# Performance work log

Hardware: AMD Instinct MI355X
Metric: run time of the kernel (lower is better)

## Reference

```python
import jax, jax.numpy as jnp
import numpy as np

NQ = 4  # n_qubits_per_head


def _apply_ry(state, theta, q):
    # state: (N, 2,2,2,2) real amplitudes; theta: (N,) per-element angle; wire q
    st = jnp.moveaxis(state, 1 + q, -1)
    c = jnp.cos(0.5 * theta).reshape(-1, 1, 1, 1)
    s = jnp.sin(0.5 * theta).reshape(-1, 1, 1, 1)
    a0, a1 = st[..., 0], st[..., 1]
    st = jnp.stack([c * a0 - s * a1, s * a0 + c * a1], axis=-1)
    return jnp.moveaxis(st, -1, 1 + q)


def _apply_cnot(state, ctrl, tgt):
    st = jnp.moveaxis(state, (1 + ctrl, 1 + tgt), (-2, -1))
    st = jnp.stack([st[..., 0, :], st[..., 1, ::-1]], axis=-2)
    return jnp.moveaxis(st, (-2, -1), (1 + ctrl, 1 + tgt))


def _quantum_circuit(x_in, par):
    # x_in: (N, NQ) data angles; par: (N, L, NQ) variational angles (per head, tiled)
    N = x_in.shape[0]
    L = par.shape[1]
    state = jnp.zeros((N, 2, 2, 2, 2), x_in.dtype).at[:, 0, 0, 0, 0].set(1.0)
    for l in range(L):
        for q in range(NQ):
            state = _apply_ry(state, par[:, l, q], q)
        for q in range(NQ - 1):
            state = _apply_cnot(state, q, q + 1)
        state = _apply_cnot(state, NQ - 1, 0)
    for q in range(NQ):
        state = _apply_ry(state, x_in[:, q], q)
    p = state * state  # probabilities (real amplitudes: only RY/CNOT gates)
    zs = []
    for q in range(NQ):
        st = jnp.moveaxis(p, 1 + q, -1)
        zs.append(jnp.sum(st[..., 0], axis=(1, 2, 3)) - jnp.sum(st[..., 1], axis=(1, 2, 3)))
    return jnp.stack(zs, axis=-1)  # (N, NQ)


def setup_inputs() -> dict:
    key = jax.random.key(0)
    ks = jax.random.split(key, 6)
    B, T, E, H, L = 4, 2048, 1024, 16, 2
    scale = 1.0 / np.sqrt(E)
    x = jax.random.normal(ks[0], (B, T, E), dtype=jnp.float32)
    Wq = jax.random.normal(ks[1], (E, E), dtype=jnp.float32) * scale
    Wk = jax.random.normal(ks[2], (E, E), dtype=jnp.float32) * scale
    Wv = jax.random.normal(ks[3], (E, E), dtype=jnp.float32) * scale
    Wo = jax.random.normal(ks[4], (E, E), dtype=jnp.float32) * scale
    qparams = jax.random.normal(ks[5], (H, L, NQ), dtype=jnp.float32)
    return {"x": x, "Wq": Wq, "Wk": Wk, "Wv": Wv, "Wo": Wo, "qparams": qparams}


def reference(x, Wq, Wk, Wv, Wo, qparams):
    B, T, E = x.shape
    H, L, _ = qparams.shape
    hd = E // H
    q = x @ Wq.T
    k = x @ Wk.T
    v = x @ Wv.T
    # NOTE: original scales by sqrt(embed_dim), not sqrt(head_dim)
    scores = jnp.einsum('bte,bse->bts', q, k) / jnp.sqrt(jnp.asarray(E, x.dtype))
    w = jax.nn.softmax(scores, axis=-1)
    out = jnp.einsum('bts,bse->bte', w, v)
    oh = out.reshape(B, T, H, hd)
    N = B * T * H
    xin = oh[..., :NQ].reshape(N, NQ)
    par = jnp.broadcast_to(qparams[None, None], (B, T, H, L, NQ)).reshape(N, L, NQ)
    z = _quantum_circuit(xin, par)  # (N, NQ)
    zfull = jnp.concatenate([z, jnp.zeros((N, hd - NQ), x.dtype)], axis=-1)
    return zfull.reshape(B, T, E) @ Wo.T
```

## Files before the change

### kernel.cpp

```cpp
#include <hip/hip_runtime.h>
#include <hip/hip_fp16.h>

typedef _Float16 half_t;
typedef __attribute__((ext_vector_type(8))) _Float16 half8;
typedef __attribute__((ext_vector_type(4))) float floatx4;

__device__ __forceinline__ void async_copy16(const void* src, void* dst_lds) {
  __builtin_amdgcn_global_load_lds(
      (__attribute__((address_space(1))) void*)src,
      (__attribute__((address_space(3))) void*)dst_lds, 16, 0, 0);
}

__global__ __launch_bounds__(512, 2) void gemm_nt_256(
    const half_t* __restrict__ A, const half_t* __restrict__ B,
    half_t* __restrict__ C,
    int lda, int ldb, int ldc, int kIters,
    long sAz2, long sBz2, long sCz2, float scale)
{
  __shared__ __align__(16) half_t sm[2][2][256 * 64];

  const int tid  = threadIdx.x;
  const int wave = tid >> 6, lane = tid & 63;
  const int wm = wave >> 2, wn = wave & 3;
  const int er = lane >> 4, ec = lane & 15;
  const int sw = ec & 7;

  const long z = blockIdx.z;
  const half_t* Ab = A + (long)blockIdx.x * 256 * lda + z * sAz2;
  const half_t* Bb = B + (long)blockIdx.y * 256 * ldb + z * sBz2;

  const int srow = tid >> 3;
  const int skq  = (tid & 7) ^ (srow & 7);

  floatx4 acc[2][2][4][2];
  #pragma unroll
  for (int a = 0; a < 2; a++)
    #pragma unroll
    for (int b = 0; b < 2; b++)
      #pragma unroll
      for (int i = 0; i < 4; i++)
        #pragma unroll
        for (int j = 0; j < 2; j++)
          acc[a][b][i][j] = (floatx4){0.f, 0.f, 0.f, 0.f};

  half8 af[4][2], bfv[2][2];
  int cur = 0;
  const int nt = kIters;

#define STAGE_A(bb, hf, kt) do {                                              \
    const half_t* Ak_ = Ab + (long)(kt) * 64;                                 \
    _Pragma("unroll")                                                         \
    for (int r_ = 0; r_ < 2; r_++) {                                          \
      int lrow_ = r_ * 64 + srow;                                             \
      async_copy16(Ak_ + (long)((hf) * 128 + lrow_) * lda + skq * 8,          \
                   &sm[(bb)][0][(hf) * 8192 + (r_ * 512 + wave * 64) * 8]);   \
    } } while (0)

#define STAGE_B(bb, hf, kt) do {                                              \
    const half_t* Bk_ = Bb + (long)(kt) * 64;                                 \
    _Pragma("unroll")                                                         \
    for (int r_ = 0; r_ < 2; r_++) {                                          \
      int lrow_ = r_ * 64 + srow;                                             \
      async_copy16(Bk_ + (long)((hf) * 128 + lrow_) * ldb + skq * 8,          \
                   &sm[(bb)][1][(hf) * 8192 + (r_ * 512 + wave * 64) * 8]);   \
    } } while (0)

#define DS_A(MH) do {                                                         \
    _Pragma("unroll")                                                         \
    for (int ii = 0; ii < 4; ii++) {                                          \
      int row_ = (MH) * 128 + wm * 64 + ii * 16 + ec;                         \
      _Pragma("unroll")                                                       \
      for (int ks = 0; ks < 2; ks++)                                          \
        af[ii][ks] = *(const half8*)                                          \
            &sm[cur][0][row_ * 64 + (((ks * 4 + er) ^ sw) * 8)];              \
    } } while (0)

#define DS_B(NH) do {                                                         \
    _Pragma("unroll")                                                         \
    for (int jj = 0; jj < 2; jj++) {                                          \
      int row_ = (NH) * 128 + wn * 32 + jj * 16 + ec;                         \
      _Pragma("unroll")                                                       \
      for (int ks = 0; ks < 2; ks++)                                          \
        bfv[jj][ks] = *(const half8*)                                         \
            &sm[cur][1][row_ * 64 + (((ks * 4 + er) ^ sw) * 8)];              \
    } } while (0)

#define MFMA_Q(MH, NH) do {                                                   \
    __builtin_amdgcn_s_setprio(1);                                            \
    _Pragma("unroll")                                                         \
    for (int ks = 0; ks < 2; ks++)                                            \
      _Pragma("unroll")                                                       \
      for (int ii = 0; ii < 4; ii++)                                          \
        _Pragma("unroll")                                                     \
        for (int jj = 0; jj < 2; jj++)                                        \
          acc[MH][NH][ii][jj] = __builtin_amdgcn_mfma_f32_16x16x32_f16(       \
              af[ii][ks], bfv[jj][ks], acc[MH][NH][ii][jj], 0, 0, 0);         \
    __builtin_amdgcn_s_setprio(0);                                            \
  } while (0)

#define BAR() __builtin_amdgcn_s_barrier()
#define LGKM0() asm volatile("s_waitcnt lgkmcnt(0)" ::: "memory")
#define VMW(N) asm volatile("s_waitcnt vmcnt(" #N ")" ::: "memory")

  STAGE_B(0, 0, 0);
  STAGE_A(0, 1, 0);
  STAGE_A(0, 0, 0);
  STAGE_B(0, 1, 0);
  if (nt > 1) {
    STAGE_B(1, 0, 1);
    STAGE_A(1, 1, 1);
    VMW(4);
  } else {
    VMW(0);
  }
  BAR();

  for (int n = 0; n < nt; ++n) {
    DS_A(0); DS_B(0);
    if (n + 1 < nt) STAGE_A(cur ^ 1, 0, n + 1);
    BAR(); LGKM0();
    MFMA_Q(0, 0);
    BAR();
    DS_A(1);
    if (n + 1 < nt) STAGE_B(cur ^ 1, 1, n + 1);
    BAR(); LGKM0();
    MFMA_Q(1, 0);
    BAR();
    DS_B(1);
    if (n + 2 < nt) STAGE_B(cur, 0, n + 2);
    BAR(); LGKM0();
    MFMA_Q(1, 1);
    BAR();
    DS_A(0);
    if (n + 2 < nt) STAGE_A(cur, 1, n + 2);
    VMW(4);
    BAR(); LGKM0();
    MFMA_Q(0, 1);
    BAR();
    cur ^= 1;
  }

#undef STAGE_A
#undef STAGE_B
#undef DS_A
#undef DS_B
#undef MFMA_Q
#undef BAR
#undef LGKM0
#undef VMW

  const long rowBase = (long)blockIdx.x * 256;
  const long colBase = (long)blockIdx.y * 256;
  half_t* Cz = C + z * sCz2;
  #pragma unroll
  for (int mh = 0; mh < 2; mh++)
    #pragma unroll
    for (int nh = 0; nh < 2; nh++)
      #pragma unroll
      for (int ii = 0; ii < 4; ii++)
        #pragma unroll
        for (int jj = 0; jj < 2; jj++)
          #pragma unroll
          for (int r = 0; r < 4; r++) {
            long row = rowBase + mh * 128 + wm * 64 + ii * 16 + er * 4 + r;
            long col = colBase + nh * 128 + wn * 32 + jj * 16 + ec;
            Cz[row * (long)ldc + col] =
                (_Float16)(acc[mh][nh][ii][jj][r] * scale);
          }
}

template<int BN, int EPI>
__global__ __launch_bounds__(256) void gemm_nt(
    const half_t* __restrict__ A, const half_t* __restrict__ B,
    void* __restrict__ Cout,
    int lda, int ldb, int ldc, int kIters, int zShift,
    long sAz1, long sBz1, long sCz1,
    long sAz2, long sBz2, long sCz2, float scale,
    const float* __restrict__ qab)
{
  constexpr int BM = 128;
  constexpr int WN = BN / 2;
  constexpr int AN = WN / 16;
  constexpr int RA = BM * 8 / 256;
  constexpr int RB = BN * 8 / 256;
  __shared__ __align__(16) half_t lA[BM * 64];
  __shared__ __align__(16) half_t lB[BN * 64];

  const int tid  = threadIdx.x;
  const int wave = tid >> 6, lane = tid & 63;
  const int wm = wave >> 1, wn = wave & 1;
  const int er = lane >> 4, ec = lane & 15;
  const int sw = ec & 7;

  const long z = blockIdx.z;
  const long z2 = z >> zShift;
  const long z1 = z - (z2 << zShift);
  const half_t* Ab = A + (long)blockIdx.x * BM * lda + z1 * sAz1 + z2 * sAz2;
  const half_t* Bb = B + (long)blockIdx.y * BN * ldb + z1 * sBz1 + z2 * sBz2;
  const long cz = z1 * sCz1 + z2 * sCz2;

  floatx4 acc[4][AN];
  #pragma unroll
  for (int i = 0; i < 4; i++)
    #pragma unroll
    for (int j = 0; j < AN; j++)
      acc[i][j] = (floatx4){0.f, 0.f, 0.f, 0.f};

  for (int ks = 0; ks < kIters; ++ks) {
    const half_t* Ak = Ab + ks * 64;
    const half_t* Bk = Bb + ks * 64;
    #pragma unroll
    for (int r = 0; r < RA; r++) {
      int s = r * 256 + tid;
      int row = s >> 3;
      int kq = (s & 7) ^ (row & 7);
      async_copy16(Ak + (long)row * lda + kq * 8,
                   &lA[(r * 256 + wave * 64) * 8]);
    }
    #pragma unroll
    for (int r = 0; r < RB; r++) {
      int s = r * 256 + tid;
      int row = s >> 3;
      int kq = (s & 7) ^ (row & 7);
      async_copy16(Bk + (long)row * ldb + kq * 8,
                   &lB[(r * 256 + wave * 64) * 8]);
    }
    __syncthreads();

    #pragma unroll
    for (int h = 0; h < 2; h++) {
      half8 af[4], bfv[AN];
      #pragma unroll
      for (int i = 0; i < 4; i++) {
        int row = wm * 64 + i * 16 + ec;
        af[i] = *(const half8*)&lA[row * 64 + (((h * 4 + er) ^ sw) * 8)];
      }
      #pragma unroll
      for (int j = 0; j < AN; j++) {
        int row = wn * WN + j * 16 + ec;
        bfv[j] = *(const half8*)&lB[row * 64 + (((h * 4 + er) ^ sw) * 8)];
      }
      #pragma unroll
      for (int i = 0; i < 4; i++)
        #pragma unroll
        for (int j = 0; j < AN; j++)
          acc[i][j] = __builtin_amdgcn_mfma_f32_16x16x32_f16(
              af[i], bfv[j], acc[i][j], 0, 0, 0);
    }
    __syncthreads();
  }

  const long rowBase = (long)blockIdx.x * BM + wm * 64;
  const long colBase = (long)blockIdx.y * BN + wn * WN;
  #pragma unroll
  for (int i = 0; i < 4; i++)
    #pragma unroll
    for (int j = 0; j < AN; j++)
      #pragma unroll
      for (int r = 0; r < 4; r++) {
        long row = rowBase + i * 16 + er * 4 + r;
        long col = colBase + j * 16 + ec;
        float v = acc[i][j][r];
        if constexpr (EPI == 0) {
          ((half_t*)Cout)[cz + row * (long)ldc + col] = (_Float16)(v * scale);
        } else if constexpr (EPI == 1) {
          ((half_t*)Cout)[cz + col * (long)ldc + row] = (_Float16)v;
        } else if constexpr (EPI == 2) {
          ((float*)Cout)[cz + row * (long)ldc + col] = v * scale;
        } else {
          float za = qab[2 * (int)col], zb = qab[2 * (int)col + 1];
          float zv = za * cosf(v) + zb * sinf(v);
          ((half_t*)Cout)[cz + row * (long)ldc + col] = (_Float16)zv;
        }
      }
}

__global__ __launch_bounds__(256) void softmax_rows(half_t* __restrict__ S,
                                                    int ld)
{
  const long row = blockIdx.x;
  half8* sp = (half8*)(S + row * (long)ld);
  const int t = threadIdx.x;
  const int wave = t >> 6, lane = t & 63;
  half8 hv = sp[t];
  float e[8];
  #pragma unroll
  for (int k = 0; k < 8; k++) e[k] = (float)hv[k];
  float m = e[0];
  #pragma unroll
  for (int k = 1; k < 8; k++) m = fmaxf(m, e[k]);
  #pragma unroll
  for (int o = 32; o > 0; o >>= 1) m = fmaxf(m, __shfl_xor(m, o));
  __shared__ float rmax[4], rsum[4];
  if (lane == 0) rmax[wave] = m;
  __syncthreads();
  m = fmaxf(fmaxf(rmax[0], rmax[1]), fmaxf(rmax[2], rmax[3]));
  float s = 0.f;
  #pragma unroll
  for (int k = 0; k < 8; k++) { e[k] = expf(e[k] - m); s += e[k]; }
  #pragma unroll
  for (int o = 32; o > 0; o >>= 1) s += __shfl_xor(s, o);
  if (lane == 0) rsum[wave] = s;
  __syncthreads();
  float inv = 1.f / (rsum[0] + rsum[1] + rsum[2] + rsum[3]);
  half8 o8;
  #pragma unroll
  for (int k = 0; k < 8; k++) o8[k] = (_Float16)(e[k] * inv);
  sp[t] = o8;
}

__global__ __launch_bounds__(256) void prep_all(
    const float* __restrict__ x,  const float* __restrict__ Wq,
    const float* __restrict__ Wk, const float* __restrict__ Wv,
    const float* __restrict__ Wo, const float* __restrict__ qp, int L,
    half_t* __restrict__ xh, half_t* __restrict__ Wqk,
    half_t* __restrict__ Wv4, half_t* __restrict__ Wos,
    float* __restrict__ qab)
{
  const int bid = blockIdx.x;
  if (bid < 4096) {
    long i = ((long)bid * 256 + threadIdx.x) * 8;
    float4 a = *(const float4*)(x + i);
    float4 b = *(const float4*)(x + i + 4);
    half8 h = {(_Float16)a.x, (_Float16)a.y, (_Float16)a.z, (_Float16)a.w,
               (_Float16)b.x, (_Float16)b.y, (_Float16)b.z, (_Float16)b.w};
    *(half8*)(xh + i) = h;
  } else if (bid < 5120) {
    long i = ((long)(bid - 4096) * 256 + threadIdx.x) * 8;
    int r = (int)(i >> 10);
    int e = (int)(i & 1023);
    const float* src = (r < 1024 ? Wq + (long)r * 1024
                                 : Wk + (long)(r - 1024) * 1024) + e;
    float4 a = *(const float4*)src;
    float4 b = *(const float4*)(src + 4);
    half8 h = {(_Float16)a.x, (_Float16)a.y, (_Float16)a.z, (_Float16)a.w,
               (_Float16)b.x, (_Float16)b.y, (_Float16)b.z, (_Float16)b.w};
    *(half8*)(Wqk + i) = h;
  } else if (bid < 5152) {
    long i = ((long)(bid - 5120) * 256 + threadIdx.x) * 8;
    int c = (int)(i >> 10);
    int e = (int)(i & 1023);
    const float* src = Wv + (long)(((c >> 2) << 6) | (c & 3)) * 1024 + e;
    float4 a = *(const float4*)src;
    float4 b = *(const float4*)(src + 4);
    half8 h = {(_Float16)a.x, (_Float16)a.y, (_Float16)a.z, (_Float16)a.w,
               (_Float16)b.x, (_Float16)b.y, (_Float16)b.z, (_Float16)b.w};
    *(half8*)(Wv4 + i) = h;
  } else if (bid < 5408) {
    int idx = (bid - 5152) * 256 + threadIdx.x;
    int e = idx >> 6, c = idx & 63;
    Wos[idx] = (_Float16)Wo[(long)e * 1024 + (((c >> 2) << 6) | (c & 3))];
  } else {
    int h = threadIdx.x;
    if (h >= 16) return;
    float st[16];
    #pragma unroll
    for (int i = 0; i < 16; i++) st[i] = 0.f;
    st[0] = 1.f;
    for (int l = 0; l < L; l++) {
      #pragma unroll
      for (int q = 0; q < 4; q++) {
        float th = qp[(h * L + l) * 4 + q];
        float c = cosf(0.5f * th), s = sinf(0.5f * th);
        int mq = 8 >> q;
        #pragma unroll
        for (int i = 0; i < 16; i++) {
          if ((i & mq) == 0) {
            float a0 = st[i], a1 = st[i | mq];
            st[i]      = c * a0 - s * a1;
            st[i | mq] = s * a0 + c * a1;
          }
        }
      }
      const int cm[4] = {8, 4, 2, 1};
      const int tm[4] = {4, 2, 1, 8};
      #pragma unroll
      for (int p = 0; p < 4; p++) {
        int mc = cm[p], mt = tm[p];
        #pragma unroll
        for (int i = 0; i < 16; i++) {
          if ((i & mc) != 0 && (i & mt) == 0) {
            float tv = st[i]; st[i] = st[i | mt]; st[i | mt] = tv;
          }
        }
      }
    }
    #pragma unroll
    for (int q = 0; q < 4; q++) {
      int mq = 8 >> q;
      float zc = 0.f, xc = 0.f;
      #pragma unroll
      for (int i = 0; i < 16; i++) {
        float p2 = st[i] * st[i];
        zc += ((i & mq) == 0) ? p2 : -p2;
        if ((i & mq) == 0) xc += st[i] * st[i | mq];
      }
      qab[(h * 4 + q) * 2 + 0] = zc;
      qab[(h * 4 + q) * 2 + 1] = -2.f * xc;
    }
  }
}

extern "C" void kernel_launch(void* const* d_in, const int* in_sizes, int n_in,
                              void* d_out, int out_size, void* d_ws, size_t ws_size,
                              hipStream_t stream)
{
  const float* x  = (const float*)d_in[0];
  const float* Wq = (const float*)d_in[1];
  const float* Wk = (const float*)d_in[2];
  const float* Wv = (const float*)d_in[3];
  const float* Wo = (const float*)d_in[4];
  const float* qp = (const float*)d_in[5];
  const int L = in_sizes[5] / 64;
  float* out = (float*)d_out;

  char* w = (char*)d_ws;
  size_t off = 0;
  auto alloc = [&](size_t bytes) -> void* {
    void* p = w + off;
    off = (off + bytes + 255) & ~(size_t)255;
    return p;
  };
  float*  qab  = (float*)alloc(512);
  half_t* xh   = (half_t*)alloc((size_t)8192 * 1024 * 2);
  half_t* Wqk  = (half_t*)alloc((size_t)2048 * 1024 * 2);
  half_t* Wv4  = (half_t*)alloc((size_t)64 * 1024 * 2);
  half_t* Wos  = (half_t*)alloc((size_t)1024 * 64 * 2);
  half_t* V4th = (half_t*)alloc((size_t)64 * 8192 * 2);
  half_t* Z4   = (half_t*)alloc((size_t)8192 * 64 * 2);

  half_t* QKb = (half_t*)d_out;

  int tier = (ws_size >= off + (size_t)8192 * 2048 * 2 + 256) ? 0 : 1;
  const size_t Sn = (tier == 0) ? (size_t)8192 * 2048 : (size_t)2048 * 2048;
  half_t* S = (half_t*)alloc(Sn * 2);

  prep_all<<<dim3(5409), dim3(256), 0, stream>>>(
      x, Wq, Wk, Wv, Wo, qp, L, xh, Wqk, Wv4, Wos, qab);

  gemm_nt_256<<<dim3(32, 8, 1), 512, 0, stream>>>(
      xh, Wqk, QKb, 1024, 1024, 2048, 16, 0, 0, 0, 1.f);
  gemm_nt<64, 1><<<dim3(64, 1, 1), 256, 0, stream>>>(
      xh, Wv4, V4th, 1024, 1024, 8192, 16, 0,
      0, 0, 0, 0, 0, 0, 1.f, nullptr);

  if (tier == 0) {
    gemm_nt_256<<<dim3(8, 8, 4), 512, 0, stream>>>(
        QKb, QKb + 1024, S, 2048, 2048, 2048, 16,
        (long)2048 * 2048, (long)2048 * 2048, (long)2048 * 2048, 0.03125f);
    softmax_rows<<<dim3(8192), dim3(256), 0, stream>>>(S, 2048);
    gemm_nt<64, 5><<<dim3(16, 1, 4), 256, 0, stream>>>(
        S, V4th, Z4, 2048, 8192, 64, 32, 0,
        0, 0, 0, (long)2048 * 2048, 2048, (long)2048 * 64, 1.f, qab);
  } else {
    for (int b = 0; b < 4; b++) {
      const long q0 = (long)b * 2048;
      gemm_nt<128, 0><<<dim3(16, 16, 1), 256, 0, stream>>>(
          QKb + q0 * 2048, QKb + 1024 + q0 * 2048, S,
          2048, 2048, 2048, 16, 0, 0, 0, 0, 0, 0, 0, 0.03125f, nullptr);
      softmax_rows<<<dim3(2048), dim3(256), 0, stream>>>(S, 2048);
      gemm_nt<64, 5><<<dim3(16, 1, 1), 256, 0, stream>>>(
          S, V4th + q0, Z4 + q0 * 64, 2048, 8192, 64, 32, 0,
          0, 0, 0, 0, 0, 0, 1.f, qab);
    }
  }

  gemm_nt<128, 2><<<dim3(64, 8, 1), 256, 0, stream>>>(
      Z4, Wos, out, 64, 64, 1024, 1, 0,
      0, 0, 0, 0, 0, 0, 1.f, nullptr);
}
```

Before: 242.0 us.

## Double-buffer register fragments so LDS reads overlap MFMA in GEMM main loop

Restructures the 256x256 GEMM main loop to split work by k-substep instead of by output quadrant. It keeps two sets of A/B register fragments so the LDS reads for the next MFMA batch are issued while the current batch runs, and drops the explicit lgkmcnt(0) waits. The global-to-LDS staging schedule changes from a two-tile lookahead to a simpler one-tile prefetch into the other buffer. This uses more registers, and the relaxed waits depend on the compiler inserting correct LDS dependency waits.

New measurement: 239.7 us. No clear change (-1.0%).

```diff
diff --git a/kernel.cpp b/kernel.cpp
--- a/kernel.cpp
+++ b/kernel.cpp
@@ -42,10 +42,6 @@
         #pragma unroll
         for (int j = 0; j < 2; j++)
           acc[a][b][i][j] = (floatx4){0.f, 0.f, 0.f, 0.f};
-
-  half8 af[4][2], bfv[2][2];
-  int cur = 0;
-  const int nt = kIters;
 
 #define STAGE_A(bb, hf, kt) do {                                              \
     const half_t* Ak_ = Ab + (long)(kt) * 64;                                 \
@@ -65,77 +61,69 @@
                    &sm[(bb)][1][(hf) * 8192 + (r_ * 512 + wave * 64) * 8]);   \
     } } while (0)
 
-#define DS_A(MH) do {                                                         \
+#define DS_A(DST, BB, MH, KS) do {                                            \
     _Pragma("unroll")                                                         \
     for (int ii = 0; ii < 4; ii++) {                                          \
       int row_ = (MH) * 128 + wm * 64 + ii * 16 + ec;                         \
-      _Pragma("unroll")                                                       \
-      for (int ks = 0; ks < 2; ks++)                                          \
-        af[ii][ks] = *(const half8*)                                          \
-            &sm[cur][0][row_ * 64 + (((ks * 4 + er) ^ sw) * 8)];              \
+      DST[ii] = *(const half8*)                                               \
+          &sm[BB][0][row_ * 64 + ((((KS) * 4 + er) ^ sw) * 8)];               \
     } } while (0)
 
-#define DS_B(NH) do {                                                         \
+#define DS_B(DST, BB, KS) do {                                                \
     _Pragma("unroll")                                                         \
-    for (int jj = 0; jj < 2; jj++) {                                          \
-      int row_ = (NH) * 128 + wn * 32 + jj * 16 + ec;                         \
-      _Pragma("unroll")                                                       \
-      for (int ks = 0; ks < 2; ks++)                                          \
-        bfv[jj][ks] = *(const half8*)                                         \
-            &sm[cur][1][row_ * 64 + (((ks * 4 + er) ^ sw) * 8)];              \
+    for (int nj = 0; nj < 4; nj++) {                                          \
+      int row_ = (nj >> 1) * 128 + wn * 32 + (nj & 1) * 16 + ec;              \
+      DST[nj] = *(const half8*)                                               \
+          &sm[BB][1][row_ * 64 + ((((KS) * 4 + er) ^ sw) * 8)];               \
     } } while (0)
 
-#define MFMA_Q(MH, NH) do {                                                   \
+#define MFMA16(AF, BF, MH) do {                                               \
     __builtin_amdgcn_s_setprio(1);                                            \
     _Pragma("unroll")                                                         \
-    for (int ks = 0; ks < 2; ks++)                                            \
+    for (int ii = 0; ii < 4; ii++)                                            \
       _Pragma("unroll")                                                       \
-      for (int ii = 0; ii < 4; ii++)                                          \
-        _Pragma("unroll")                                                     \
-        for (int jj = 0; jj < 2; jj++)                                        \
-          acc[MH][NH][ii][jj] = __builtin_amdgcn_mfma_f32_16x16x32_f16(       \
-              af[ii][ks], bfv[jj][ks], acc[MH][NH][ii][jj], 0, 0, 0);         \
+      for (int nj = 0; nj < 4; nj++)                                          \
+        acc[MH][nj >> 1][ii][nj & 1] =                                        \
+            __builtin_amdgcn_mfma_f32_16x16x32_f16(                           \
+                AF[ii], BF[nj], acc[MH][nj >> 1][ii][nj & 1], 0, 0, 0);       \
     __builtin_amdgcn_s_setprio(0);                                            \
   } while (0)
 
 #define BAR() __builtin_amdgcn_s_barrier()
-#define LGKM0() asm volatile("s_waitcnt lgkmcnt(0)" ::: "memory")
 #define VMW(N) asm volatile("s_waitcnt vmcnt(" #N ")" ::: "memory")
 
-  STAGE_B(0, 0, 0);
-  STAGE_A(0, 1, 0);
-  STAGE_A(0, 0, 0);
-  STAGE_B(0, 1, 0);
-  if (nt > 1) {
-    STAGE_B(1, 0, 1);
-    STAGE_A(1, 1, 1);
-    VMW(4);
-  } else {
-    VMW(0);
-  }
+  half8 afA[4], afB[4], bfA[4], bfB[4];
+  int cur = 0;
+  const int nt = kIters;
+
+  STAGE_B(0, 0, 0); STAGE_B(0, 1, 0); STAGE_A(0, 0, 0); STAGE_A(0, 1, 0);
+  VMW(2);
   BAR();
+  DS_A(afA, 0, 0, 0);
+  DS_B(bfA, 0, 0);
 
   for (int n = 0; n < nt; ++n) {
-    DS_A(0); DS_B(0);
-    if (n + 1 < nt) STAGE_A(cur ^ 1, 0, n + 1);
-    BAR(); LGKM0();
-    MFMA_Q(0, 0);
+    const int hasNext = (n + 1 < nt);
+    DS_A(afB, cur, 0, 1);
+    DS_B(bfB, cur, 1);
+    if (hasNext) { STAGE_B(cur ^ 1, 0, n + 1); STAGE_B(cur ^ 1, 1, n + 1); }
+    MFMA16(afA, bfA, 0);
+    if (hasNext) { VMW(4); } else { VMW(0); }
     BAR();
-    DS_A(1);
-    if (n + 1 < nt) STAGE_B(cur ^ 1, 1, n + 1);
-    BAR(); LGKM0();
-    MFMA_Q(1, 0);
+    DS_A(afA, cur, 1, 0);
+    if (hasNext) STAGE_A(cur ^ 1, 0, n + 1);
+    MFMA16(afB, bfB, 0);
     BAR();
-    DS_B(1);
-    if (n + 2 < nt) STAGE_B(cur, 0, n + 2);
-    BAR(); LGKM0();
-    MFMA_Q(1, 1);
+    DS_A(afB, cur, 1, 1);
+    if (hasNext) STAGE_A(cur ^ 1, 1, n + 1);
+    MFMA16(afA, bfA, 1);
+    if (hasNext) VMW(2);
     BAR();
-    DS_A(0);
-    if (n + 2 < nt) STAGE_A(cur, 1, n + 2);
-    VMW(4);
-    BAR(); LGKM0();
-    MFMA_Q(0, 1);
+    if (hasNext) {
+      DS_A(afA, cur ^ 1, 0, 0);
+      DS_B(bfA, cur ^ 1, 0);
+    }
+    MFMA16(afB, bfB, 1);
     BAR();
     cur ^= 1;
   }
@@ -144,9 +132,8 @@
 #undef STAGE_B
 #undef DS_A
 #undef DS_B
-#undef MFMA_Q
+#undef MFMA16
 #undef BAR
-#undef LGKM0
 #undef VMW
 
   const long rowBase = (long)blockIdx.x * 256;
```
